# Optimization experiments

Hardware: AMD Instinct MI355X
Metric: run time of the kernel (lower is better)

Reference implementation:

```python
import jax, jax.numpy as jnp
import numpy as np

H = 768
NH = 12
HD = H // NH  # 64


def setup_inputs() -> dict:
    key = jax.random.key(0)
    ks = jax.random.split(key, 8)
    B, S = 4, 2048
    sc = 1.0 / np.sqrt(H)
    return {
        "hidden_states": jax.random.normal(ks[0], (B, S, H), dtype=jnp.float32),
        "attention_mask": jnp.zeros((B, 1, 1, S), dtype=jnp.float32),
        "Wq": jax.random.normal(ks[1], (H, H), dtype=jnp.float32) * sc,
        "bq": jnp.zeros((H,), dtype=jnp.float32),
        "Wk": jax.random.normal(ks[2], (H, H), dtype=jnp.float32) * sc,
        "bk": jnp.zeros((H,), dtype=jnp.float32),
        "Wv": jax.random.normal(ks[3], (H, H), dtype=jnp.float32) * sc,
        "bv": jnp.zeros((H,), dtype=jnp.float32),
    }


def _split_heads(x):
    # [B,S,H] -> [B,NH,S,HD]
    B, S, _ = x.shape
    return x.reshape(B, S, NH, HD).transpose(0, 2, 1, 3)


def reference(hidden_states, attention_mask, Wq, bq, Wk, bk, Wv, bv):
    q = _split_heads(hidden_states @ Wq + bq)
    k = _split_heads(hidden_states @ Wk + bk)
    v = _split_heads(hidden_states @ Wv + bv)
    # scores: [B,NH,S,S]
    scores = jnp.einsum("bhqd,bhkd->bhqk", q, k) / np.sqrt(HD)
    scores = scores + attention_mask
    probs = jax.nn.softmax(scores, axis=-1)  # dropout is identity in eval
    ctx = jnp.einsum("bhqk,bhkd->bhqd", probs, v)
    B, _, S, _ = ctx.shape
    return ctx.transpose(0, 2, 1, 3).reshape(B, S, H)
```

## Files before the change

kernel.cpp:

```cpp
#include <hip/hip_runtime.h>
#include <stdint.h>

typedef short bf16x8 __attribute__((ext_vector_type(8)));
typedef float f32x4  __attribute__((ext_vector_type(4)));
typedef float f32x16 __attribute__((ext_vector_type(16)));
typedef unsigned short u16;

#define B_  4
#define S_  2048
#define H_  768
#define NH_ 12
#define HD_ 64
#define NPROJ_N (3*H_)

static __device__ __forceinline__ u16 f2bf(float f) {
    union { float f; unsigned int u; } x; x.f = f;
    return (u16)((x.u + 0x8000u) >> 16);
}
static __device__ __forceinline__ bf16x8 ld8(const u16* p) {
    return *(const bf16x8*)(const void*)p;
}
static __device__ __forceinline__ void st8(u16* p, bf16x8 v) {
    *(bf16x8*)(void*)p = v;
}
static __device__ __forceinline__ void async_ld16(const u16* g, const short* l) {
    __builtin_amdgcn_global_load_lds(
        (__attribute__((address_space(1))) void*)g,
        (__attribute__((address_space(3))) void*)l,
        16, 0, 0);
}
static __device__ __forceinline__ unsigned cvtpk(float a, float b) {
    unsigned r;
    asm("v_cvt_pk_bf16_f32 %0, %1, %2" : "=v"(r) : "v"(a), "v"(b));
    return r;
}
static __device__ __forceinline__ void pl32swap(unsigned& a, unsigned& b) {
    asm("v_permlane32_swap_b32 %0, %1" : "+v"(a), "+v"(b));
}
static __device__ __forceinline__ bf16x8 mk8(unsigned a, unsigned b, unsigned c, unsigned d) {
    union { unsigned u[4]; bf16x8 v; } x;
    x.u[0] = a; x.u[1] = b; x.u[2] = c; x.u[3] = d;
    return x.v;
}

__global__ __launch_bounds__(256) void prep_kernel(const float* __restrict__ in,
                                                   u16* __restrict__ out,
                                                   const float* __restrict__ wq,
                                                   const float* __restrict__ wk,
                                                   const float* __restrict__ wv,
                                                   u16* __restrict__ wt,
                                                   const float* __restrict__ amask,
                                                   float* __restrict__ msc) {
    __shared__ float t[32][33];
    const int blk = blockIdx.x;
    const int tid = threadIdx.x;
    if (blk < 6144) {
        int i = (blk * 256 + tid) * 4;
        float4 v = *(const float4*)(in + i);
        ushort4 o;
        o.x = f2bf(v.x); o.y = f2bf(v.y); o.z = f2bf(v.z); o.w = f2bf(v.w);
        *(ushort4*)(out + i) = o;
    } else if (blk < 7872) {
        const int idx  = blk - 6144;
        const int proj = idx / 576;
        const int rem  = idx % 576;
        const int bx = rem % 24, by = rem / 24;
        const float* w = (proj == 0) ? wq : (proj == 1) ? wk : wv;
        u16* o = wt + (size_t)proj * H_ * H_;
        const int tx = tid & 31, ty = tid >> 5;
        const int n0 = bx * 32, k0 = by * 32;
        #pragma unroll
        for (int i = 0; i < 4; i++)
            t[ty + i * 8][tx] = w[(size_t)(k0 + ty + i * 8) * H_ + n0 + tx];
        __syncthreads();
        #pragma unroll
        for (int i = 0; i < 4; i++)
            o[(size_t)(n0 + ty + i * 8) * H_ + k0 + tx] = f2bf(t[tx][ty + i * 8]);
    } else {
        const int i = ((blk - 7872) * 256 + tid) * 8;
        float4 a0 = *(const float4*)(amask + i);
        float4 a1 = *(const float4*)(amask + i + 4);
        a0.x *= 1.44269504f; a0.y *= 1.44269504f; a0.z *= 1.44269504f; a0.w *= 1.44269504f;
        a1.x *= 1.44269504f; a1.y *= 1.44269504f; a1.z *= 1.44269504f; a1.w *= 1.44269504f;
        *(float4*)(msc + i)     = a0;
        *(float4*)(msc + i + 4) = a1;
    }
}

__global__ __launch_bounds__(256) void qkv_gemm(const u16* __restrict__ A,
                                                const u16* __restrict__ Wt,
                                                const float* __restrict__ bq,
                                                const float* __restrict__ bk,
                                                const float* __restrict__ bv,
                                                u16* __restrict__ qo,
                                                u16* __restrict__ ko,
                                                u16* __restrict__ vto) {
    __shared__ alignas(16) short SMEM[4][128 * 64];

    const int tid  = threadIdx.x;
    const int wave = tid >> 6;
    const int lane = tid & 63;
    const int quad = lane >> 4;
    const int l16  = lane & 15;
    const int wm   = wave & 1;
    const int wn   = wave >> 1;

    const int id  = blockIdx.x;
    const int xcd = id & 7;
    const int j   = id >> 3;
    const int mi  = j & 7;
    const int ni  = j >> 3;
    const int m0 = (xcd * 8 + mi) * 128;
    const int n0 = ni * 128;

    int stR[4], stC[4];
    #pragma unroll
    for (int jj = 0; jj < 4; jj++) {
        const int lc = wave * 256 + jj * 64 + lane;
        stR[jj] = lc >> 3;
        stC[jj] = ((lc & 7) ^ (stR[jj] & 7)) * 8;
    }
    const int fx0 = (quad ^ (l16 & 7)) * 8;
    const int fx1 = fx0 ^ 32;

    f32x4 acc[4][4];
    #pragma unroll
    for (int i = 0; i < 4; i++)
        #pragma unroll
        for (int jj = 0; jj < 4; jj++) acc[i][jj] = (f32x4)0.0f;

#define GSTAGE(kt_, buf_)                                                                     \
    do {                                                                                      \
        const int kk_ = (kt_) * 64;                                                           \
        _Pragma("unroll")                                                                     \
        for (int jj = 0; jj < 4; jj++) {                                                      \
            async_ld16(A  + (size_t)(m0 + stR[jj]) * H_ + kk_ + stC[jj],                      \
                       &SMEM[(buf_) * 2][(wave * 256 + jj * 64) * 8]);                        \
            async_ld16(Wt + (size_t)(n0 + stR[jj]) * H_ + kk_ + stC[jj],                      \
                       &SMEM[(buf_) * 2 + 1][(wave * 256 + jj * 64) * 8]);                    \
        }                                                                                     \
    } while (0)

    GSTAGE(0, 0);
    __syncthreads();

    for (int kt = 0; kt < 12; kt++) {
        const int cur = kt & 1;
        if (kt + 1 < 12) GSTAGE(kt + 1, cur ^ 1);
        const short* As = SMEM[cur * 2];
        const short* Bs = SMEM[cur * 2 + 1];
        #pragma unroll
        for (int ks = 0; ks < 2; ks++) {
            const int fx = ks ? fx1 : fx0;
            bf16x8 af[4], bfr[4];
            #pragma unroll
            for (int i = 0; i < 4; i++)
                af[i] = *(const bf16x8*)(const void*)&As[(wm * 64 + i * 16 + l16) * 64 + fx];
            #pragma unroll
            for (int jj = 0; jj < 4; jj++)
                bfr[jj] = *(const bf16x8*)(const void*)&Bs[(wn * 64 + jj * 16 + l16) * 64 + fx];
            #pragma unroll
            for (int i = 0; i < 4; i++)
                #pragma unroll
                for (int jj = 0; jj < 4; jj++)
                    acc[i][jj] = __builtin_amdgcn_mfma_f32_16x16x32_bf16(af[i], bfr[jj], acc[i][jj], 0, 0, 0);
        }
        __syncthreads();
    }
#undef GSTAGE

    const int proj  = n0 / H_;
    const int hbase = (n0 % H_) >> 6;
    const float* bias = (proj == 0) ? bq : (proj == 1) ? bk : bv;
    u16* Ct = (u16*)SMEM;

    #pragma unroll
    for (int nj = 0; nj < 4; nj++) {
        const int nl = wn * 64 + nj * 16 + l16;
        const float bv_ = bias[(n0 % H_) + nl];
        #pragma unroll
        for (int mi2 = 0; mi2 < 4; mi2++) {
            #pragma unroll
            for (int r = 0; r < 4; r++) {
                const int ml = wm * 64 + mi2 * 16 + quad * 4 + r;
                const u16 val = f2bf(acc[mi2][nj][r] + bv_);
                if (proj < 2)
                    Ct[ml * 128 + ((nl + (ml & 15) * 8) & 127)] = val;
                else
                    Ct[nl * 128 + ((ml + (nl & 15) * 8) & 127)] = val;
            }
        }
    }
    __syncthreads();

    if (proj < 2) {
        u16* dst0 = (proj == 0) ? qo : ko;
        const int c = tid & 7;
        #pragma unroll
        for (int jj = 0; jj < 8; jj++) {
            const int idx = jj * 32 + (tid >> 3);
            const int ml = idx >> 1, h2 = idx & 1;
            const int nbase = h2 * 64 + c * 8;
            bf16x8 v8 = *(const bf16x8*)(const void*)&Ct[ml * 128 + ((nbase + (ml & 15) * 8) & 127)];
            const int m = m0 + ml;
            const int b = m >> 11, s = m & 2047;
            st8(dst0 + ((size_t)(b * NH_ + hbase + h2) * S_ + s) * HD_ + c * 8, v8);
        }
    } else {
        const int b = m0 >> 11;
        #pragma unroll
        for (int jj = 0; jj < 8; jj++) {
            const int nl = (tid >> 3) + (jj & 3) * 32;
            const int c  = (tid & 7) + (jj >> 2) * 8;
            bf16x8 v8 = *(const bf16x8*)(const void*)&Ct[nl * 128 + ((c * 8 + (nl & 15) * 8) & 127)];
            const int h2 = nl >> 6, d = nl & 63;
            st8(vto + ((size_t)(b * NH_ + hbase + h2) * HD_ + d) * S_ + (m0 & 2047) + c * 8, v8);
        }
    }
}

__global__ __launch_bounds__(256, 3) void attn_kernel(const u16* __restrict__ q,
                                                      const u16* __restrict__ k,
                                                      const u16* __restrict__ vt,
                                                      const float* __restrict__ msc,
                                                      float* __restrict__ out) {
    __shared__ alignas(16) short Ks[2][4096];
    __shared__ alignas(16) short Vs[2][4096];
    __shared__ alignas(16) float Ms[S_];

    const int tid  = threadIdx.x;
    const int wave = tid >> 6;
    const int lane = tid & 63;
    const int l32  = lane & 31;
    const int h    = lane >> 5;
    const int kh   = wave & 1;
    const int qg   = wave >> 1;

    const int bh = blockIdx.x;
    const int b  = bh / NH_;
    const int q0 = blockIdx.y * 128;
    const float C1 = 0.125f * 1.44269504f;

    {
        const float* mrow = msc + (size_t)b * S_;
        float4 a0 = *(const float4*)(mrow + tid * 8);
        float4 a1 = *(const float4*)(mrow + tid * 8 + 4);
        *(float4*)(Ms + tid * 8)     = a0;
        *(float4*)(Ms + tid * 8 + 4) = a1;
    }

    bf16x8 qf[2][4];
    #pragma unroll
    for (int qb = 0; qb < 2; qb++) {
        const u16* qrow = q + ((size_t)bh * S_ + q0 + qg * 64 + qb * 32 + l32) * HD_;
        #pragma unroll
        for (int i = 0; i < 4; i++) qf[qb][i] = ld8(qrow + i * 16 + h * 8);
    }

    const u16* kbase = k  + (size_t)bh * S_ * HD_;
    const u16* vbase = vt + (size_t)bh * HD_ * S_;

    const int sRow = tid >> 3;
    const int sCol = ((tid & 7) ^ (sRow & 7)) * 8;
    const int rx   = l32 & 7;

    float ls0 = 0.f, ls1 = 0.f;
    f32x16 oacc[2][2];
    #pragma unroll
    for (int qb = 0; qb < 2; qb++)
        #pragma unroll
        for (int dh = 0; dh < 2; dh++) oacc[qb][dh] = (f32x16)0.0f;

#define STAGE(kt_, buf_)                                                                           \
    do {                                                                                           \
        async_ld16(kbase + (size_t)(kt_) * 4096 + sRow * 64 + sCol,          &Ks[buf_][tid * 8]);  \
        async_ld16(kbase + (size_t)(kt_) * 4096 + (sRow + 32) * 64 + sCol,   &Ks[buf_][2048 + tid * 8]); \
        async_ld16(vbase + (size_t)sRow * S_ + (kt_) * 64 + sCol,            &Vs[buf_][tid * 8]);  \
        async_ld16(vbase + (size_t)(sRow + 32) * S_ + (kt_) * 64 + sCol,     &Vs[buf_][2048 + tid * 8]); \
    } while (0)

    STAGE(0, 0);
    __syncthreads();

    for (int kt = 0; kt < S_ / 64; kt++) {
        const int cur = kt & 1;
        if (kt + 1 < S_ / 64) STAGE(kt + 1, cur ^ 1);
        const short* Kc = Ks[cur];
        const short* Vc = Vs[cur];

        f32x16 s0 = (f32x16)0.0f;
        f32x16 s1 = (f32x16)0.0f;
        __builtin_amdgcn_s_setprio(1);
        #pragma unroll
        for (int i = 0; i < 4; i++) {
            bf16x8 kf = *(const bf16x8*)(const void*)&Kc[kh * 2048 + l32 * 64 + (((h + 2 * i) ^ rx) * 8)];
            s0 = __builtin_amdgcn_mfma_f32_32x32x16_bf16(kf, qf[0][i], s0, 0, 0, 0);
            s1 = __builtin_amdgcn_mfma_f32_32x32x16_bf16(kf, qf[1][i], s1, 0, 0, 0);
        }
        __builtin_amdgcn_s_setprio(0);

        unsigned w0[8], w1[8];
        #pragma unroll
        for (int c = 0; c < 4; c++) {
            const f32x4 mm = *(const f32x4*)&Ms[kt * 64 + kh * 32 + c * 8 + h * 4];
            const float p00 = __builtin_amdgcn_exp2f(__builtin_fmaf(s0[4*c+0], C1, mm[0]));
            const float p01 = __builtin_amdgcn_exp2f(__builtin_fmaf(s0[4*c+1], C1, mm[1]));
            const float p02 = __builtin_amdgcn_exp2f(__builtin_fmaf(s0[4*c+2], C1, mm[2]));
            const float p03 = __builtin_amdgcn_exp2f(__builtin_fmaf(s0[4*c+3], C1, mm[3]));
            const float p10 = __builtin_amdgcn_exp2f(__builtin_fmaf(s1[4*c+0], C1, mm[0]));
            const float p11 = __builtin_amdgcn_exp2f(__builtin_fmaf(s1[4*c+1], C1, mm[1]));
            const float p12 = __builtin_amdgcn_exp2f(__builtin_fmaf(s1[4*c+2], C1, mm[2]));
            const float p13 = __builtin_amdgcn_exp2f(__builtin_fmaf(s1[4*c+3], C1, mm[3]));
            w0[2*c]   = cvtpk(p00, p01);
            w0[2*c+1] = cvtpk(p02, p03);
            w1[2*c]   = cvtpk(p10, p11);
            w1[2*c+1] = cvtpk(p12, p13);
            ls0 += (p00 + p01) + (p02 + p03);
            ls1 += (p10 + p11) + (p12 + p13);
        }

        bf16x8 pa0[2], pa1[2];
        #pragma unroll
        for (int t = 0; t < 2; t++) {
            {
                unsigned a = w0[4*t+0], bb = w0[4*t+2];
                pl32swap(a, bb);
                unsigned c2 = w0[4*t+1], dd = w0[4*t+3];
                pl32swap(c2, dd);
                pa0[t] = mk8(a, c2, bb, dd);
            }
            {
                unsigned a = w1[4*t+0], bb = w1[4*t+2];
                pl32swap(a, bb);
                unsigned c2 = w1[4*t+1], dd = w1[4*t+3];
                pl32swap(c2, dd);
                pa1[t] = mk8(a, c2, bb, dd);
            }
        }

        __builtin_amdgcn_s_setprio(1);
        #pragma unroll
        for (int t = 0; t < 2; t++) {
            #pragma unroll
            for (int dh = 0; dh < 2; dh++) {
                bf16x8 vf = *(const bf16x8*)(const void*)&Vc[dh * 2048 + l32 * 64 + (((kh * 4 + 2 * t + h) ^ rx) * 8)];
                oacc[0][dh] = __builtin_amdgcn_mfma_f32_32x32x16_bf16(pa0[t], vf, oacc[0][dh], 0, 0, 0);
                oacc[1][dh] = __builtin_amdgcn_mfma_f32_32x32x16_bf16(pa1[t], vf, oacc[1][dh], 0, 0, 0);
            }
        }
        __builtin_amdgcn_s_setprio(0);
        __syncthreads();
    }
#undef STAGE

    ls0 += __shfl_xor(ls0, 32);
    ls1 += __shfl_xor(ls1, 32);

    float* R = qg ? (float*)Vs : (float*)Ks;

    if (kh == 1) {
        #pragma unroll
        for (int qb = 0; qb < 2; qb++)
            #pragma unroll
            for (int dh = 0; dh < 2; dh++)
                #pragma unroll
                for (int r = 0; r < 16; r++) {
                    const int qrow = (r & 3) + 8 * (r >> 2) + 4 * h;
                    R[(qb * 32 + qrow) * 64 + dh * 32 + l32] = oacc[qb][dh][r];
                }
        if (lane < 32) {
            Ms[qg * 64 + l32]      = ls0;
            Ms[qg * 64 + 32 + l32] = ls1;
        }
    }
    __syncthreads();

    if (kh == 0) {
        const float li0 = 1.0f / (ls0 + Ms[qg * 64 + l32]);
        const float li1 = 1.0f / (ls1 + Ms[qg * 64 + 32 + l32]);
        const int hh = bh % NH_;
        #pragma unroll
        for (int r = 0; r < 16; r++) {
            const int qrow = (r & 3) + 8 * (r >> 2) + 4 * h;
            const float lv0 = __shfl(li0, qrow);
            const float lv1 = __shfl(li1, qrow);
            #pragma unroll
            for (int dh = 0; dh < 2; dh++) {
                const int d = dh * 32 + l32;
                const int s0r = q0 + qg * 64 + qrow;
                out[((size_t)b * S_ + s0r) * H_ + hh * 64 + d] =
                    (oacc[0][dh][r] + R[qrow * 64 + d]) * lv0;
                out[((size_t)b * S_ + s0r + 32) * H_ + hh * 64 + d] =
                    (oacc[1][dh][r] + R[(32 + qrow) * 64 + d]) * lv1;
            }
        }
    }
}

extern "C" void kernel_launch(void* const* d_in, const int* in_sizes, int n_in,
                              void* d_out, int out_size, void* d_ws, size_t ws_size,
                              hipStream_t stream) {
    const float* hidden = (const float*)d_in[0];
    const float* amask  = (const float*)d_in[1];
    const float* Wq     = (const float*)d_in[2];
    const float* bq     = (const float*)d_in[3];
    const float* Wk     = (const float*)d_in[4];
    const float* bk     = (const float*)d_in[5];
    const float* Wv     = (const float*)d_in[6];
    const float* bv     = (const float*)d_in[7];
    float* out = (float*)d_out;

    char* ws = (char*)d_ws;
    const size_t sz_hidden = (size_t)B_ * S_ * H_ * 2;
    const size_t sz_wt     = (size_t)NPROJ_N * H_ * 2;
    const size_t sz_qkv    = (size_t)B_ * S_ * H_ * 2;

    u16* hid_bf = (u16*)(ws);
    u16* wt     = (u16*)(ws + sz_hidden);
    u16* qbuf   = (u16*)(ws + sz_hidden + sz_wt);
    u16* kbuf   = (u16*)(ws + sz_hidden + sz_wt + sz_qkv);
    u16* vtbuf  = (u16*)(ws + sz_hidden + sz_wt + 2 * sz_qkv);
    float* msc  = (float*)(ws + sz_hidden + sz_wt + 3 * sz_qkv);

    prep_kernel<<<dim3(6144 + 1728 + 4), dim3(256), 0, stream>>>(
        hidden, hid_bf, Wq, Wk, Wv, wt, amask, msc);
    qkv_gemm<<<dim3(1152), dim3(256), 0, stream>>>(
        hid_bf, wt, bq, bk, bv, qbuf, kbuf, vtbuf);
    attn_kernel<<<dim3(B_ * NH_, S_ / 128), dim3(256), 0, stream>>>(
        qbuf, kbuf, vtbuf, msc, out);
}
```

Baseline: 204.2 us.

## Software-pipeline QK^T of next tile with softmax-PV of current tile

Splits the attention inner loop into a QK^T stage and a softmax+PV stage, and computes the scores for tile kt+1 before processing tile kt so that the MFMA work can overlap the exp/pack work. K gets triple buffering and V keeps double buffering, with the K prefetch issued two tiles ahead. This adds LDS for a third K buffer and keeps two extra f32x16 score accumulators live, which raises register pressure and could reduce occupancy under launch bounds of 3 blocks per CU.

```diff
diff --git a/kernel.cpp b/kernel.cpp
--- a/kernel.cpp
+++ b/kernel.cpp
@@ -224,7 +224,7 @@
                                                       const u16* __restrict__ vt,
                                                       const float* __restrict__ msc,
                                                       float* __restrict__ out) {
-    __shared__ alignas(16) short Ks[2][4096];
+    __shared__ alignas(16) short Ks[3][4096];
     __shared__ alignas(16) short Vs[2][4096];
     __shared__ alignas(16) float Ms[S_];
 
@@ -271,25 +271,20 @@
         #pragma unroll
         for (int dh = 0; dh < 2; dh++) oacc[qb][dh] = (f32x16)0.0f;
 
-#define STAGE(kt_, buf_)                                                                           \
+#define STAGE_K(kt_, bi_)                                                                          \
     do {                                                                                           \
-        async_ld16(kbase + (size_t)(kt_) * 4096 + sRow * 64 + sCol,          &Ks[buf_][tid * 8]);  \
-        async_ld16(kbase + (size_t)(kt_) * 4096 + (sRow + 32) * 64 + sCol,   &Ks[buf_][2048 + tid * 8]); \
-        async_ld16(vbase + (size_t)sRow * S_ + (kt_) * 64 + sCol,            &Vs[buf_][tid * 8]);  \
-        async_ld16(vbase + (size_t)(sRow + 32) * S_ + (kt_) * 64 + sCol,     &Vs[buf_][2048 + tid * 8]); \
+        async_ld16(kbase + (size_t)(kt_) * 4096 + sRow * 64 + sCol,        &Ks[bi_][tid * 8]);     \
+        async_ld16(kbase + (size_t)(kt_) * 4096 + (sRow + 32) * 64 + sCol, &Ks[bi_][2048 + tid * 8]); \
     } while (0)
-
-    STAGE(0, 0);
-    __syncthreads();
-
-    for (int kt = 0; kt < S_ / 64; kt++) {
-        const int cur = kt & 1;
-        if (kt + 1 < S_ / 64) STAGE(kt + 1, cur ^ 1);
-        const short* Kc = Ks[cur];
-        const short* Vc = Vs[cur];
-
-        f32x16 s0 = (f32x16)0.0f;
-        f32x16 s1 = (f32x16)0.0f;
+#define STAGE_V(kt_, bi_)                                                                          \
+    do {                                                                                           \
+        async_ld16(vbase + (size_t)sRow * S_ + (kt_) * 64 + sCol,          &Vs[bi_][tid * 8]);     \
+        async_ld16(vbase + (size_t)(sRow + 32) * S_ + (kt_) * 64 + sCol,   &Vs[bi_][2048 + tid * 8]); \
+    } while (0)
+
+    auto qk = [&](const short* Kc, f32x16& s0, f32x16& s1) {
+        s0 = (f32x16)0.0f;
+        s1 = (f32x16)0.0f;
         __builtin_amdgcn_s_setprio(1);
         #pragma unroll
         for (int i = 0; i < 4; i++) {
@@ -298,7 +293,9 @@
             s1 = __builtin_amdgcn_mfma_f32_32x32x16_bf16(kf, qf[1][i], s1, 0, 0, 0);
         }
         __builtin_amdgcn_s_setprio(0);
-
+    };
+
+    auto smpv = [&](int kt, const short* Vc, const f32x16& s0, const f32x16& s1) {
         unsigned w0[8], w1[8];
         #pragma unroll
         for (int c = 0; c < 4; c++) {
@@ -349,9 +346,28 @@
             }
         }
         __builtin_amdgcn_s_setprio(0);
+    };
+
+    STAGE_K(0, 0);
+    STAGE_K(1, 1);
+    STAGE_V(0, 0);
+    __syncthreads();
+
+    f32x16 sc0, sc1, sn0, sn1;
+    qk(Ks[0], sc0, sc1);
+
+    for (int kt = 0; kt < 31; kt++) {
+        if (kt + 2 < 32) STAGE_K(kt + 2, (kt + 2) % 3);
+        STAGE_V(kt + 1, (kt + 1) & 1);
+        qk(Ks[(kt + 1) % 3], sn0, sn1);
+        smpv(kt, Vs[kt & 1], sc0, sc1);
         __syncthreads();
-    }
-#undef STAGE
+        sc0 = sn0; sc1 = sn1;
+    }
+    smpv(31, Vs[1], sc0, sc1);
+    __syncthreads();
+#undef STAGE_K
+#undef STAGE_V
 
     ls0 += __shfl_xor(ls0, 32);
     ls1 += __shfl_xor(ls1, 32);
```

After: 249.8 us. 1.22x slower.
